# Optimization experiments

Measured on AMD Instinct MI355X. Metric: run time of the kernel, lower is better.

## Reference

```python
import math
import jax, jax.numpy as jnp
import numpy as np

N = 50000   # nodes
E = 200000  # edges
B = 1024    # graphs
D = 256     # d_model
DA = 128    # d_atom_embed
DB = 64     # d_bond_embed
NA = 16     # num_atom_types
NB = 5      # num_bond_types
L = 6       # num_layers
DC = 2      # d_cond
IN0 = DA + 8 + D  # 392, layer-0 input dim


def setup_inputs() -> dict:
    key = jax.random.key(0)
    ks = jax.random.split(key, 48)
    def w(i, shape):
        fan_in = shape[-2] if len(shape) >= 2 else shape[-1]
        return jax.random.normal(ks[i], shape, jnp.float32) / jnp.sqrt(jnp.float32(fan_in))
    inp = {
        'x_noisy': jax.random.randint(ks[0], (N,), 0, NA),
        'node_mask_obs': jax.random.randint(ks[1], (N,), 0, 2),
        'edge_attr_noisy': jax.random.randint(ks[2], (E,), 0, NB),
        'edge_mask_obs': jax.random.randint(ks[3], (E,), 0, 2),
        'edge_index': jax.random.randint(ks[4], (2, E), 0, N),
        't_node': jax.random.randint(ks[5], (N,), 0, 200),
        'cond_vec': jax.random.normal(ks[6], (B, DC), jnp.float32),
        'batch': jnp.sort(jax.random.randint(ks[7], (N,), 0, B)),
        # embeddings
        'atom_emb': w(8, (NA, DA)), 'bond_emb': w(9, (NB, DB)),
        'nmask_emb': w(10, (2, 8)), 'emask_emb': w(11, (2, 8)),
        # timestep MLP
        't_W1': w(12, (D, D)), 't_b1': jnp.zeros((D,)),
        't_W2': w(13, (D, D)), 't_b2': jnp.zeros((D,)),
        # cond projection
        'cond_W': w(14, (DC, D)), 'cond_b': jnp.zeros((D,)),
        # edge MLP
        'edge_W1': w(15, (DB + 8, D)), 'edge_b1': jnp.zeros((D,)),
        'edge_W2': w(16, (D, D)), 'edge_b2': jnp.zeros((D,)),
        # layer-0 edge projection (GINEConv edge_dim -> in_dim)
        'e0_W': w(17, (D, IN0)),
        # layer-0 GINEConv MLP
        'conv0_W1': w(18, (IN0, D)), 'conv0_b1': jnp.zeros((D,)),
        'conv0_W2': w(19, (D, D)), 'conv0_b2': jnp.zeros((D,)),
        'conv0_eps': jnp.zeros(()),
        # layers 1..5 GINEConv MLPs (stacked)
        'convs_W1': w(20, (L - 1, D, D)), 'convs_b1': jnp.zeros((L - 1, D)),
        'convs_W2': w(21, (L - 1, D, D)), 'convs_b2': jnp.zeros((L - 1, D)),
        'convs_eps': jnp.zeros((L - 1,)),
        # BatchNorm (eval mode: running_mean=0, running_var=1)
        'bn_gamma': jnp.ones((L, D)) + 0.1 * jax.random.normal(ks[22], (L, D), jnp.float32),
        'bn_beta': 0.1 * jax.random.normal(ks[23], (L, D), jnp.float32),
        # heads
        'atom_W': w(24, (D, NA)), 'atom_b': jnp.zeros((NA,)),
        'bond_W': w(25, (D, NB)), 'bond_b': jnp.zeros((NB,)),
    }
    return inp


def _sinusoidal(t, d_model):
    half = d_model // 2
    freqs = jnp.exp(jnp.arange(half, dtype=jnp.float32) * (-math.log(10000.0) / max(1, half - 1)))
    angles = t.astype(jnp.float32)[:, None] * freqs[None, :]
    return jnp.concatenate([jnp.sin(angles), jnp.cos(angles)], axis=1)


def _bn_eval(h, gamma, beta, eps=1e-5):
    # running_mean=0, running_var=1
    return h * (gamma / jnp.sqrt(1.0 + eps)) + beta


def reference(x_noisy, node_mask_obs, edge_attr_noisy, edge_mask_obs, edge_index,
              t_node, cond_vec, batch,
              atom_emb, bond_emb, nmask_emb, emask_emb,
              t_W1, t_b1, t_W2, t_b2, cond_W, cond_b,
              edge_W1, edge_b1, edge_W2, edge_b2, e0_W,
              conv0_W1, conv0_b1, conv0_W2, conv0_b2, conv0_eps,
              convs_W1, convs_b1, convs_W2, convs_b2, convs_eps,
              bn_gamma, bn_beta, atom_W, atom_b, bond_W, bond_b):
    silu = jax.nn.silu
    # node features
    x_atom = atom_emb[x_noisy]                       # [N, DA]
    x_mask = nmask_emb[node_mask_obs]                # [N, 8]
    t_emb = _sinusoidal(t_node, D)                   # [N, D]
    t_emb = silu(t_emb @ t_W1 + t_b1) @ t_W2 + t_b2
    c_node = (cond_vec @ cond_W + cond_b)[batch]     # [N, D]
    h = jnp.concatenate([x_atom, x_mask, t_emb + c_node], axis=-1)  # [N, IN0]
    # edge features
    e_in = jnp.concatenate([bond_emb[edge_attr_noisy], emask_emb[edge_mask_obs]], axis=-1)
    e_feat = silu(e_in @ edge_W1 + edge_b1) @ edge_W2 + edge_b2      # [E, D]
    src, dst = edge_index[0], edge_index[1]

    def gine(h, e, eps, W1, b1, W2, b2):
        msg = jax.nn.relu(h[src] + e)                               # [E, d]
        agg = jax.ops.segment_sum(msg, dst, num_segments=N)          # [N, d]
        z = (1.0 + eps) * h + agg
        return silu(z @ W1 + b1) @ W2 + b2

    # layer 0 (edge features projected to IN0)
    h = gine(h, e_feat @ e0_W, conv0_eps, conv0_W1, conv0_b1, conv0_W2, conv0_b2)
    h = silu(_bn_eval(h, bn_gamma[0], bn_beta[0]))  # dropout off (eval)
    # layers 1..5
    for i in range(L - 1):
        h = gine(h, e_feat, convs_eps[i], convs_W1[i], convs_b1[i], convs_W2[i], convs_b2[i])
        h = silu(_bn_eval(h, bn_gamma[i + 1], bn_beta[i + 1]))
    atom_logits = h @ atom_W + atom_b                # [N, NA]
    edge_h = h[src] + h[dst]                          # [E, D]
    bond_logits = edge_h @ bond_W + bond_b            # [E, NB]
    return atom_logits, bond_logits
```

## Files before the change

### kernel.cpp

```cpp
#include <hip/hip_runtime.h>
#include <cstdint>
#include <cmath>

typedef unsigned short u16;
typedef unsigned int   u32;

using bf16x8 = __attribute__((ext_vector_type(8))) short;
using f32x4  = __attribute__((ext_vector_type(4))) float;

#define DM 256
#define W0 448
#define W0_REAL 392

__device__ __forceinline__ float bf2f(u16 v) {
  union { u32 u; float f; } c; c.u = ((u32)v) << 16; return c.f;
}
__device__ __forceinline__ u16 f2bf(float f) {
  union { float f; u32 u; } c; c.f = f;
  u32 u = c.u;
  return (u16)((u + 0x7FFFu + ((u >> 16) & 1u)) >> 16);
}
__device__ __forceinline__ float siluf(float y) {
  return y / (1.0f + __expf(-y));
}
__device__ __forceinline__ uint4 pack8(float f0, float f1, float f2, float f3,
                                       float f4, float f5, float f6, float f7) {
  uint4 o;
  o.x = (u32)f2bf(f0) | ((u32)f2bf(f1) << 16);
  o.y = (u32)f2bf(f2) | ((u32)f2bf(f3) << 16);
  o.z = (u32)f2bf(f4) | ((u32)f2bf(f5) << 16);
  o.w = (u32)f2bf(f6) | ((u32)f2bf(f7) << 16);
  return o;
}
__device__ __forceinline__ void acc8(float4& lo, float4& hi, uint4 hv,
                                     float4 ea, float4 eb) {
  lo.x += fmaxf(bf2f((u16)(hv.x & 0xFFFF)) + ea.x, 0.f);
  lo.y += fmaxf(bf2f((u16)(hv.x >> 16))    + ea.y, 0.f);
  lo.z += fmaxf(bf2f((u16)(hv.y & 0xFFFF)) + ea.z, 0.f);
  lo.w += fmaxf(bf2f((u16)(hv.y >> 16))    + ea.w, 0.f);
  hi.x += fmaxf(bf2f((u16)(hv.z & 0xFFFF)) + eb.x, 0.f);
  hi.y += fmaxf(bf2f((u16)(hv.z >> 16))    + eb.y, 0.f);
  hi.z += fmaxf(bf2f((u16)(hv.w & 0xFFFF)) + eb.z, 0.f);
  hi.w += fmaxf(bf2f((u16)(hv.w >> 16))    + eb.w, 0.f);
}
__device__ __forceinline__ void g2l16(const u16* g, u16* l) {
  __builtin_amdgcn_global_load_lds(
      (__attribute__((address_space(1))) u32*)g,
      (__attribute__((address_space(3))) u32*)l, 16, 0, 0);
}

__global__ void wT_kernel(const float* __restrict__ W, u16* __restrict__ out,
                          int nmat, int K, int Kpad, int Nc) {
  int idx = blockIdx.x * 256 + threadIdx.x;
  int tot = nmat * Nc * Kpad;
  if (idx >= tot) return;
  int m = idx / (Nc * Kpad);
  int r = idx - m * (Nc * Kpad);
  int n = r / Kpad;
  int k = r - n * Kpad;
  float v = (k < K) ? W[(size_t)m * K * Nc + (size_t)k * Nc + n] : 0.0f;
  out[idx] = f2bf(v);
}

__global__ void whead_kernel(const float* __restrict__ atomW, const float* __restrict__ bondW,
                             u16* __restrict__ out) {
  int idx = blockIdx.x * 256 + threadIdx.x;
  if (idx >= 32 * 256) return;
  int j = idx >> 8, k = idx & 255;
  float v = 0.0f;
  if (j < 16) v = atomW[k * 16 + j];
  else if (j < 21) v = bondW[k * 5 + (j - 16)];
  out[idx] = f2bf(v);
}

__global__ void t_table_kernel(const float* __restrict__ W1, const float* __restrict__ b1,
                               const float* __restrict__ W2, const float* __restrict__ b2,
                               float* __restrict__ out) {
  __shared__ float s[256];
  __shared__ float a1[256];
  int r = blockIdx.x, t = threadIdx.x;
  float tv = (float)r;
  float coef = -logf(10000.0f) / 127.0f;
  int j = t & 127;
  float ang = tv * expf(coef * (float)j);
  s[t] = (t < 128) ? sinf(ang) : cosf(ang);
  __syncthreads();
  float acc = b1[t];
  for (int k = 0; k < 256; ++k) acc = fmaf(s[k], W1[k * 256 + t], acc);
  a1[t] = acc / (1.0f + expf(-acc));
  __syncthreads();
  float acc2 = b2[t];
  for (int k = 0; k < 256; ++k) acc2 = fmaf(a1[k], W2[k * 256 + t], acc2);
  out[r * 256 + t] = acc2;
}

__global__ void cproj_kernel(const float* __restrict__ cv, const float* __restrict__ W,
                             const float* __restrict__ b, float* __restrict__ out, int B) {
  int i = blockIdx.x * 256 + threadIdx.x;
  if (i < B * 256) {
    int g = i >> 8, c = i & 255;
    out[i] = fmaf(cv[g * 2], W[c], fmaf(cv[g * 2 + 1], W[256 + c], b[c]));
  }
}

__global__ void ef_tab_kernel(const float* __restrict__ bond_emb, const float* __restrict__ emask_emb,
                              const float* __restrict__ W1, const float* __restrict__ b1,
                              const float* __restrict__ W2, const float* __restrict__ b2,
                              float* __restrict__ out) {
  __shared__ float ein[72];
  __shared__ float a1[256];
  int bidx = blockIdx.x;
  int bt = bidx >> 1, m = bidx & 1;
  int t = threadIdx.x;
  if (t < 64) ein[t] = bond_emb[bt * 64 + t];
  else if (t < 72) ein[t] = emask_emb[m * 8 + (t - 64)];
  __syncthreads();
  float acc = b1[t];
  for (int k = 0; k < 72; ++k) acc = fmaf(ein[k], W1[k * 256 + t], acc);
  a1[t] = acc / (1.0f + expf(-acc));
  __syncthreads();
  float acc2 = b2[t];
  for (int k = 0; k < 256; ++k) acc2 = fmaf(a1[k], W2[k * 256 + t], acc2);
  out[bidx * 256 + t] = acc2;
}

__global__ void e0_tab_kernel(const float* __restrict__ eftab, const float* __restrict__ e0W,
                              float* __restrict__ out) {
  __shared__ float ef[256];
  int bidx = blockIdx.x, t = threadIdx.x;
  if (t < 256) ef[t] = eftab[bidx * 256 + t];
  __syncthreads();
  if (t < W0) {
    float acc = 0.0f;
    if (t < W0_REAL) {
      for (int k = 0; k < 256; ++k) acc = fmaf(ef[k], e0W[k * W0_REAL + t], acc);
    }
    out[bidx * W0 + t] = acc;
  }
}

__global__ void h0_kernel(const int* __restrict__ x, const int* __restrict__ nm,
                          const int* __restrict__ tnode, const int* __restrict__ batch,
                          const float* __restrict__ atom_emb, const float* __restrict__ nmask_emb,
                          const float* __restrict__ ttab, const float* __restrict__ cproj,
                          u16* __restrict__ h0, int N) {
  int idx = blockIdx.x * 256 + threadIdx.x;
  if (idx >= N * 56) return;
  int n = idx / 56;
  int ch = idx - n * 56;
  uint4 o;
  if (ch < 16) {
    const float* s = atom_emb + (size_t)x[n] * 128 + ch * 8;
    float4 a = *(const float4*)s, b = *(const float4*)(s + 4);
    o = pack8(a.x, a.y, a.z, a.w, b.x, b.y, b.z, b.w);
  } else if (ch == 16) {
    const float* s = nmask_emb + (size_t)nm[n] * 8;
    float4 a = *(const float4*)s, b = *(const float4*)(s + 4);
    o = pack8(a.x, a.y, a.z, a.w, b.x, b.y, b.z, b.w);
  } else if (ch < 49) {
    int cc = ch * 8 - 136;
    const float* ta = ttab + (size_t)tnode[n] * 256 + cc;
    const float* cb = cproj + (size_t)batch[n] * 256 + cc;
    float4 a = *(const float4*)ta, b = *(const float4*)(ta + 4);
    float4 c = *(const float4*)cb, d = *(const float4*)(cb + 4);
    o = pack8(a.x + c.x, a.y + c.y, a.z + c.z, a.w + c.w,
              b.x + d.x, b.y + d.y, b.z + d.z, b.w + d.w);
  } else {
    o = make_uint4(0, 0, 0, 0);
  }
  *(uint4*)(h0 + (size_t)n * W0 + ch * 8) = o;
}

__global__ void deg_kernel(const int* __restrict__ dst, int* __restrict__ deg, int E) {
  int e = blockIdx.x * 256 + threadIdx.x;
  if (e < E) atomicAdd(&deg[dst[e]], 1);
}

__global__ void scan1_kernel(const int* __restrict__ deg, int* __restrict__ ro,
                             int* __restrict__ bsum, int N) {
  __shared__ int tmp[256];
  int tid = threadIdx.x, i = blockIdx.x * 256 + tid;
  int v = (i < N) ? deg[i] : 0;
  tmp[tid] = v;
  __syncthreads();
  for (int o = 1; o < 256; o <<= 1) {
    int t = (tid >= o) ? tmp[tid - o] : 0;
    __syncthreads();
    tmp[tid] += t;
    __syncthreads();
  }
  if (i < N) ro[i] = tmp[tid] - v;
  if (tid == 255) bsum[blockIdx.x] = tmp[255];
}

__global__ void scan2_kernel(int* __restrict__ bsum, int nb) {
  __shared__ int tmp[256];
  int tid = threadIdx.x;
  int v = (tid < nb) ? bsum[tid] : 0;
  tmp[tid] = v;
  __syncthreads();
  for (int o = 1; o < 256; o <<= 1) {
    int t = (tid >= o) ? tmp[tid - o] : 0;
    __syncthreads();
    tmp[tid] += t;
    __syncthreads();
  }
  if (tid < nb) bsum[tid] = tmp[tid] - v;
}

__global__ void scan3_kernel(int* __restrict__ ro, int* __restrict__ cur,
                             const int* __restrict__ bsum, int N, int E) {
  int i = blockIdx.x * 256 + threadIdx.x;
  if (i < N) {
    int r = ro[i] + bsum[blockIdx.x];
    ro[i] = r;
    cur[i] = r;
  }
  if (i == 0) ro[N] = E;
}

__global__ void fill_kernel(const int* __restrict__ src, const int* __restrict__ dst,
                            const int* __restrict__ ea, const int* __restrict__ em,
                            int* __restrict__ cur, int* __restrict__ csr, int E) {
  int e = blockIdx.x * 256 + threadIdx.x;
  if (e < E) {
    int d = dst[e];
    int pos = atomicAdd(&cur[d], 1);
    csr[pos] = src[e] | ((ea[e] * 2 + em[e]) << 20);
  }
}

__global__ __launch_bounds__(256) void agg_z256(
    const u16* __restrict__ h, const float* __restrict__ etab,
    const int* __restrict__ ro, const int* __restrict__ csr,
    const float* __restrict__ epsp, u16* __restrict__ z, int N) {
  int wid = threadIdx.x >> 6, lane = threadIdx.x & 63;
  int n = blockIdx.x * 4 + wid;
  if (n >= N) return;
  int s0 = ro[n], s1 = ro[n + 1];
  float eps1 = 1.0f + *epsp;
  int half = lane >> 5, li = lane & 31;
  int c8 = li * 8;
  float4 aLo = {0, 0, 0, 0}, aHi = {0, 0, 0, 0};

  for (int base = s0; base < s1; base += 64) {
    int m = s1 - base; if (m > 64) m = 64;
    int pk = (lane < m) ? csr[base + lane] : 0;
    int j = 0;
    for (; j + 7 < m; j += 8) {
      int p0 = __shfl(pk, j + half);
      int p1 = __shfl(pk, j + 2 + half);
      int p2 = __shfl(pk, j + 4 + half);
      int p3 = __shfl(pk, j + 6 + half);
      uint4 h0v = *(const uint4*)(h + (size_t)(p0 & 0xFFFFF) * 256 + c8);
      uint4 h1v = *(const uint4*)(h + (size_t)(p1 & 0xFFFFF) * 256 + c8);
      uint4 h2v = *(const uint4*)(h + (size_t)(p2 & 0xFFFFF) * 256 + c8);
      uint4 h3v = *(const uint4*)(h + (size_t)(p3 & 0xFFFFF) * 256 + c8);
      const float* e0p = etab + (size_t)(p0 >> 20) * 256 + c8;
      const float* e1p = etab + (size_t)(p1 >> 20) * 256 + c8;
      const float* e2p = etab + (size_t)(p2 >> 20) * 256 + c8;
      const float* e3p = etab + (size_t)(p3 >> 20) * 256 + c8;
      float4 e0a = *(const float4*)e0p, e0b = *(const float4*)(e0p + 4);
      float4 e1a = *(const float4*)e1p, e1b = *(const float4*)(e1p + 4);
      float4 e2a = *(const float4*)e2p, e2b = *(const float4*)(e2p + 4);
      float4 e3a = *(const float4*)e3p, e3b = *(const float4*)(e3p + 4);
      acc8(aLo, aHi, h0v, e0a, e0b);
      acc8(aLo, aHi, h1v, e1a, e1b);
      acc8(aLo, aHi, h2v, e2a, e2b);
      acc8(aLo, aHi, h3v, e3a, e3b);
    }
    for (; j < m; j += 2) {
      int idx = j + half;
      bool act = idx < m;
      int p = __shfl(pk, act ? idx : (m - 1));
      uint4 hv = *(const uint4*)(h + (size_t)(p & 0xFFFFF) * 256 + c8);
      const float* ep = etab + (size_t)(p >> 20) * 256 + c8;
      float4 ea = *(const float4*)ep, eb = *(const float4*)(ep + 4);
      if (act) acc8(aLo, aHi, hv, ea, eb);
    }
  }
  aLo.x += __shfl(aLo.x, li + 32); aLo.y += __shfl(aLo.y, li + 32);
  aLo.z += __shfl(aLo.z, li + 32); aLo.w += __shfl(aLo.w, li + 32);
  aHi.x += __shfl(aHi.x, li + 32); aHi.y += __shfl(aHi.y, li + 32);
  aHi.z += __shfl(aHi.z, li + 32); aHi.w += __shfl(aHi.w, li + 32);
  if (half == 0) {
    uint4 hn = *(const uint4*)(h + (size_t)n * 256 + c8);
    uint4 o = pack8(
        eps1 * bf2f((u16)(hn.x & 0xFFFF)) + aLo.x,
        eps1 * bf2f((u16)(hn.x >> 16))    + aLo.y,
        eps1 * bf2f((u16)(hn.y & 0xFFFF)) + aLo.z,
        eps1 * bf2f((u16)(hn.y >> 16))    + aLo.w,
        eps1 * bf2f((u16)(hn.z & 0xFFFF)) + aHi.x,
        eps1 * bf2f((u16)(hn.z >> 16))    + aHi.y,
        eps1 * bf2f((u16)(hn.w & 0xFFFF)) + aHi.z,
        eps1 * bf2f((u16)(hn.w >> 16))    + aHi.w);
    *(uint4*)(z + (size_t)n * 256 + c8) = o;
  }
}

__global__ __launch_bounds__(256) void agg_z448(
    const u16* __restrict__ h, const float* __restrict__ etab,
    const int* __restrict__ ro, const int* __restrict__ csr,
    const float* __restrict__ epsp, u16* __restrict__ z, int N) {
  int wid = threadIdx.x >> 6, lane = threadIdx.x & 63;
  int n = blockIdx.x * 4 + wid;
  if (n >= N) return;
  int s0 = ro[n], s1 = ro[n + 1];
  float eps1 = 1.0f + *epsp;
  bool live = lane < 56;
  int c8 = live ? lane * 8 : 440;
  float4 aLo = {0, 0, 0, 0}, aHi = {0, 0, 0, 0};

  for (int base = s0; base < s1; base += 64) {
    int m = s1 - base; if (m > 64) m = 64;
    int pk = (lane < m) ? csr[base + lane] : 0;
    int j = 0;
    for (; j + 3 < m; j += 4) {
      int p0 = __shfl(pk, j);
      int p1 = __shfl(pk, j + 1);
      int p2 = __shfl(pk, j + 2);
      int p3 = __shfl(pk, j + 3);
      uint4 h0v = *(const uint4*)(h + (size_t)(p0 & 0xFFFFF) * W0 + c8);
      uint4 h1v = *(const uint4*)(h + (size_t)(p1 & 0xFFFFF) * W0 + c8);
      uint4 h2v = *(const uint4*)(h + (size_t)(p2 & 0xFFFFF) * W0 + c8);
      uint4 h3v = *(const uint4*)(h + (size_t)(p3 & 0xFFFFF) * W0 + c8);
      const float* e0p = etab + (size_t)(p0 >> 20) * W0 + c8;
      const float* e1p = etab + (size_t)(p1 >> 20) * W0 + c8;
      const float* e2p = etab + (size_t)(p2 >> 20) * W0 + c8;
      const float* e3p = etab + (size_t)(p3 >> 20) * W0 + c8;
      float4 e0a = *(const float4*)e0p, e0b = *(const float4*)(e0p + 4);
      float4 e1a = *(const float4*)e1p, e1b = *(const float4*)(e1p + 4);
      float4 e2a = *(const float4*)e2p, e2b = *(const float4*)(e2p + 4);
      float4 e3a = *(const float4*)e3p, e3b = *(const float4*)(e3p + 4);
      acc8(aLo, aHi, h0v, e0a, e0b);
      acc8(aLo, aHi, h1v, e1a, e1b);
      acc8(aLo, aHi, h2v, e2a, e2b);
      acc8(aLo, aHi, h3v, e3a, e3b);
    }
    for (; j < m; ++j) {
      int p = __shfl(pk, j);
      uint4 hv = *(const uint4*)(h + (size_t)(p & 0xFFFFF) * W0 + c8);
      const float* ep = etab + (size_t)(p >> 20) * W0 + c8;
      float4 ea = *(const float4*)ep, eb = *(const float4*)(ep + 4);
      acc8(aLo, aHi, hv, ea, eb);
    }
  }
  if (live) {
    uint4 hn = *(const uint4*)(h + (size_t)n * W0 + c8);
    uint4 o = pack8(
        eps1 * bf2f((u16)(hn.x & 0xFFFF)) + aLo.x,
        eps1 * bf2f((u16)(hn.x >> 16))    + aLo.y,
        eps1 * bf2f((u16)(hn.y & 0xFFFF)) + aLo.z,
        eps1 * bf2f((u16)(hn.y >> 16))    + aLo.w,
        eps1 * bf2f((u16)(hn.z & 0xFFFF)) + aHi.x,
        eps1 * bf2f((u16)(hn.z >> 16))    + aHi.y,
        eps1 * bf2f((u16)(hn.w & 0xFFFF)) + aHi.z,
        eps1 * bf2f((u16)(hn.w >> 16))    + aHi.w);
    *(uint4*)(z + (size_t)n * W0 + c8) = o;
  }
}

__global__ __launch_bounds__(256, 3) void gemm_fused(
    const u16* __restrict__ A, const u16* __restrict__ BT,
    const float* __restrict__ bias, const float* __restrict__ scale,
    const float* __restrict__ shift, u16* __restrict__ C, int M, int K) {
  __shared__ __align__(16) u16 smem[20480];
  u16* lA = smem;
  u16* lB = smem + 4096;
  int tid = threadIdx.x;
  int wid = tid >> 6, lane = tid & 63;
  int q = lane >> 4, rr = lane & 15;
  int wm = wid >> 1, wn = wid & 1;
  int m0 = blockIdx.x * 64;
  int lr8 = lane >> 3;
  int swz = (lane & 7) ^ (lr8 & 7);

  f32x4 acc[2][8] = {};

  for (int k0 = 0; k0 < K; k0 += 64) {
#pragma unroll
    for (int p = 0; p < 2; ++p) {
      int idx = wid * 2 + p;
      int gr = m0 + idx * 8 + lr8;
      if (gr >= M) gr = M - 1;
      g2l16(A + (size_t)gr * K + k0 + swz * 8, lA + idx * 512);
    }
#pragma unroll
    for (int p = 0; p < 8; ++p) {
      int idx = wid * 8 + p;
      int nr = idx * 8 + lr8;
      g2l16(BT + (size_t)nr * K + k0 + swz * 8, lB + idx * 512);
    }
    __syncthreads();
#pragma unroll
    for (int ks = 0; ks < 2; ++ks) {
      int slot = ((ks * 4 + q) ^ (rr & 7)) << 3;
      bf16x8 af[2], bfv[8];
#pragma unroll
      for (int mt = 0; mt < 2; ++mt)
        af[mt] = *(const bf16x8*)&lA[(wm * 32 + mt * 16 + rr) * 64 + slot];
#pragma unroll
      for (int nt = 0; nt < 8; ++nt)
        bfv[nt] = *(const bf16x8*)&lB[(wn * 128 + nt * 16 + rr) * 64 + slot];
#pragma unroll
      for (int mt = 0; mt < 2; ++mt)
#pragma unroll
        for (int nt = 0; nt < 8; ++nt)
          acc[mt][nt] = __builtin_amdgcn_mfma_f32_16x16x32_bf16(af[mt], bfv[nt], acc[mt][nt], 0, 0, 0);
    }
    __syncthreads();
  }

  u16* lC = smem;
#pragma unroll
  for (int nt = 0; nt < 8; ++nt) {
    int c = wn * 128 + nt * 16 + rr;
    float b = bias[c];
    float sc = scale ? scale[c] * 0.9999950000374997f : 1.0f;
    float sh = shift ? shift[c] : 0.0f;
#pragma unroll
    for (int mt = 0; mt < 2; ++mt)
#pragma unroll
      for (int i = 0; i < 4; ++i) {
        int r = wm * 32 + mt * 16 + q * 4 + i;
        float y = (acc[mt][nt][i] + b) * sc + sh;
        lC[r * 256 + c] = f2bf(siluf(y));
      }
  }
  __syncthreads();
#pragma unroll
  for (int it = 0; it < 8; ++it) {
    int idx = it * 256 + tid;
    int r = idx >> 5, c16 = idx & 31;
    if (m0 + r < M)
      *(uint4*)(C + (size_t)(m0 + r) * 256 + c16 * 8) =
          *(const uint4*)(lC + r * 256 + c16 * 8);
  }
}

__global__ __launch_bounds__(256) void head_gemm(
    const u16* __restrict__ A, const u16* __restrict__ WT,
    const float* __restrict__ atomB,
    float* __restrict__ atom_out, float* __restrict__ P, int M) {
  __shared__ __align__(16) u16 lA[128 * 32];
  __shared__ __align__(16) u16 lB[32 * 264];
  int tid = threadIdx.x;
  int wid = tid >> 6, lane = tid & 63;
  int q = lane >> 4, rr = lane & 15;
  int m0 = blockIdx.x * 128;

  for (int i = tid; i < 32 * 256; i += 256)
    lB[(i >> 8) * 264 + (i & 255)] = WT[i];

  f32x4 acc[2][2] = {};
  int arow = tid >> 2, acol = (tid & 3) * 8;

  for (int k0 = 0; k0 < 256; k0 += 32) {
#pragma unroll
    for (int p = 0; p < 2; ++p) {
      int gr = m0 + p * 64 + arow;
      if (gr >= M) gr = M - 1;
      g2l16(A + (size_t)gr * 256 + k0 + acol, &lA[p * 2048 + wid * 512]);
    }
    __syncthreads();
    bf16x8 af[2], bfr[2];
#pragma unroll
    for (int mt = 0; mt < 2; ++mt)
      af[mt] = *(const bf16x8*)&lA[(wid * 32 + mt * 16 + rr) * 32 + q * 8];
#pragma unroll
    for (int nt = 0; nt < 2; ++nt)
      bfr[nt] = *(const bf16x8*)&lB[(nt * 16 + rr) * 264 + k0 + q * 8];
#pragma unroll
    for (int mt = 0; mt < 2; ++mt)
#pragma unroll
      for (int nt = 0; nt < 2; ++nt)
        acc[mt][nt] = __builtin_amdgcn_mfma_f32_16x16x32_bf16(af[mt], bfr[nt], acc[mt][nt], 0, 0, 0);
    __syncthreads();
  }

#pragma unroll
  for (int nt = 0; nt < 2; ++nt) {
    int c = nt * 16 + rr;
    float bb = (c < 16) ? atomB[c] : 0.0f;
#pragma unroll
    for (int mt = 0; mt < 2; ++mt) {
      int rbase = m0 + wid * 32 + mt * 16 + q * 4;
#pragma unroll
      for (int r2 = 0; r2 < 4; ++r2) {
        int row = rbase + r2;
        if (row < M) {
          float v = acc[mt][nt][r2];
          if (c < 16) atom_out[(size_t)row * 16 + c] = v + bb;
          else if (c < 21) P[(size_t)row * 8 + (c - 16)] = v;
        }
      }
    }
  }
}

__global__ __launch_bounds__(256) void bond_edge(
    const float* __restrict__ P, const int* __restrict__ src,
    const int* __restrict__ dst, const float* __restrict__ b,
    float* __restrict__ out, int E) {
  __shared__ float so[256 * 5];
  int t = threadIdx.x;
  int e = blockIdx.x * 256 + t;
  float v0 = 0, v1 = 0, v2 = 0, v3 = 0, v4 = 0;
  if (e < E) {
    int s = src[e], d = dst[e];
    float4 ps = *(const float4*)(P + (size_t)s * 8);
    float  p4s = P[(size_t)s * 8 + 4];
    float4 pd = *(const float4*)(P + (size_t)d * 8);
    float  p4d = P[(size_t)d * 8 + 4];
    v0 = ps.x + pd.x + b[0];
    v1 = ps.y + pd.y + b[1];
    v2 = ps.z + pd.z + b[2];
    v3 = ps.w + pd.w + b[3];
    v4 = p4s + p4d + b[4];
  }
  so[t * 5 + 0] = v0; so[t * 5 + 1] = v1; so[t * 5 + 2] = v2;
  so[t * 5 + 3] = v3; so[t * 5 + 4] = v4;
  __syncthreads();
  size_t base = (size_t)blockIdx.x * 256 * 5;
  size_t lim = (size_t)E * 5;
  for (int i = t; i < 256 * 5; i += 256) {
    size_t g = base + i;
    if (g < lim) out[g] = so[i];
  }
}

extern "C" void kernel_launch(void* const* d_in, const int* in_sizes, int n_in,
                              void* d_out, int out_size, void* d_ws, size_t ws_size,
                              hipStream_t stream) {
  const int*   x_noisy   = (const int*)d_in[0];
  const int*   nmaskobs  = (const int*)d_in[1];
  const int*   ea        = (const int*)d_in[2];
  const int*   em        = (const int*)d_in[3];
  const int*   eidx      = (const int*)d_in[4];
  const int*   tnode     = (const int*)d_in[5];
  const float* cvec      = (const float*)d_in[6];
  const int*   batch     = (const int*)d_in[7];
  const float* atom_emb  = (const float*)d_in[8];
  const float* bond_emb  = (const float*)d_in[9];
  const float* nmask_emb = (const float*)d_in[10];
  const float* emask_emb = (const float*)d_in[11];
  const float* t_W1      = (const float*)d_in[12];
  const float* t_b1      = (const float*)d_in[13];
  const float* t_W2      = (const float*)d_in[14];
  const float* t_b2      = (const float*)d_in[15];
  const float* cond_W    = (const float*)d_in[16];
  const float* cond_b    = (const float*)d_in[17];
  const float* edge_W1   = (const float*)d_in[18];
  const float* edge_b1   = (const float*)d_in[19];
  const float* edge_W2   = (const float*)d_in[20];
  const float* edge_b2   = (const float*)d_in[21];
  const float* e0_W      = (const float*)d_in[22];
  const float* conv0_W1  = (const float*)d_in[23];
  const float* conv0_b1  = (const float*)d_in[24];
  const float* conv0_W2  = (const float*)d_in[25];
  const float* conv0_b2  = (const float*)d_in[26];
  const float* conv0_eps = (const float*)d_in[27];
  const float* convs_W1  = (const float*)d_in[28];
  const float* convs_b1  = (const float*)d_in[29];
  const float* convs_W2  = (const float*)d_in[30];
  const float* convs_b2  = (const float*)d_in[31];
  const float* convs_eps = (const float*)d_in[32];
  const float* bn_gamma  = (const float*)d_in[33];
  const float* bn_beta   = (const float*)d_in[34];
  const float* atom_W    = (const float*)d_in[35];
  const float* atom_b    = (const float*)d_in[36];
  const float* bond_W    = (const float*)d_in[37];
  const float* bond_b    = (const float*)d_in[38];

  const int N = in_sizes[0];
  const int E = in_sizes[2];
  const int B = in_sizes[6] / 2;
  const int* srcp = eidx;
  const int* dstp = eidx + E;

  char* base = (char*)d_ws;
  size_t off = 0;
  auto alloc = [&](size_t bytes) -> char* {
    char* p = base + off;
    off = (off + bytes + 255) & ~(size_t)255;
    return p;
  };
  u16* h0   = (u16*)alloc((size_t)N * W0 * 2);
  u16* z0   = (u16*)alloc((size_t)N * W0 * 2);
  u16* ubuf = (u16*)alloc((size_t)N * DM * 2);
  u16* w10t = (u16*)alloc((size_t)DM * W0 * 2);
  u16* w20t = (u16*)alloc((size_t)DM * DM * 2);
  u16* wc1t = (u16*)alloc((size_t)5 * DM * DM * 2);
  u16* wc2t = (u16*)alloc((size_t)5 * DM * DM * 2);
  u16* wht  = (u16*)alloc((size_t)32 * DM * 2);
  float* ttab  = (float*)alloc((size_t)200 * DM * 4);
  float* cprojb= (float*)alloc((size_t)B * DM * 4);
  float* eftab = (float*)alloc((size_t)10 * DM * 4);
  float* e0tab = (float*)alloc((size_t)10 * W0 * 4);
  float* Pbuf  = (float*)alloc((size_t)N * 8 * 4);
  int* deg  = (int*)alloc((size_t)N * 4);
  int* ro   = (int*)alloc((size_t)(N + 1) * 4);
  int* cur  = (int*)alloc((size_t)N * 4);
  int* csr  = (int*)alloc((size_t)E * 4);
  int* bsum = (int*)alloc((size_t)256 * 4);
  (void)ws_size; (void)n_in; (void)out_size;

  u16* hbuf = h0;
  u16* zbuf = z0;
  float* atom_out = (float*)d_out;
  float* bond_out = atom_out + (size_t)N * 16;

  hipMemsetAsync(deg, 0, (size_t)N * 4, stream);

  wT_kernel<<<(DM * W0 + 255) / 256, 256, 0, stream>>>(conv0_W1, w10t, 1, W0_REAL, W0, DM);
  wT_kernel<<<(DM * DM + 255) / 256, 256, 0, stream>>>(conv0_W2, w20t, 1, DM, DM, DM);
  wT_kernel<<<(5 * DM * DM + 255) / 256, 256, 0, stream>>>(convs_W1, wc1t, 5, DM, DM, DM);
  wT_kernel<<<(5 * DM * DM + 255) / 256, 256, 0, stream>>>(convs_W2, wc2t, 5, DM, DM, DM);
  whead_kernel<<<32, 256, 0, stream>>>(atom_W, bond_W, wht);
  t_table_kernel<<<200, 256, 0, stream>>>(t_W1, t_b1, t_W2, t_b2, ttab);
  cproj_kernel<<<(B * DM + 255) / 256, 256, 0, stream>>>(cvec, cond_W, cond_b, cprojb, B);
  ef_tab_kernel<<<10, 256, 0, stream>>>(bond_emb, emask_emb, edge_W1, edge_b1, edge_W2, edge_b2, eftab);
  e0_tab_kernel<<<10, 512, 0, stream>>>(eftab, e0_W, e0tab);
  h0_kernel<<<(N * 56 + 255) / 256, 256, 0, stream>>>(x_noisy, nmaskobs, tnode, batch,
      atom_emb, nmask_emb, ttab, cprojb, h0, N);
  const int nscan = (N + 255) / 256;
  deg_kernel<<<(E + 255) / 256, 256, 0, stream>>>(dstp, deg, E);
  scan1_kernel<<<nscan, 256, 0, stream>>>(deg, ro, bsum, N);
  scan2_kernel<<<1, 256, 0, stream>>>(bsum, nscan);
  scan3_kernel<<<nscan, 256, 0, stream>>>(ro, cur, bsum, N, E);
  fill_kernel<<<(E + 255) / 256, 256, 0, stream>>>(srcp, dstp, ea, em, cur, csr, E);

  const int ggrid = (N + 63) / 64;
  const int nagg = (N + 3) / 4;
  agg_z448<<<nagg, 256, 0, stream>>>(h0, e0tab, ro, csr, conv0_eps, z0, N);
  gemm_fused<<<ggrid, 256, 0, stream>>>(z0, w10t, conv0_b1, nullptr, nullptr, ubuf, N, W0);
  gemm_fused<<<ggrid, 256, 0, stream>>>(ubuf, w20t, conv0_b2, bn_gamma, bn_beta, hbuf, N, DM);
  for (int i = 0; i < 5; ++i) {
    agg_z256<<<nagg, 256, 0, stream>>>(hbuf, eftab, ro, csr, convs_eps + i, zbuf, N);
    gemm_fused<<<ggrid, 256, 0, stream>>>(zbuf, wc1t + (size_t)i * DM * DM, convs_b1 + i * DM,
                                          nullptr, nullptr, ubuf, N, DM);
    gemm_fused<<<ggrid, 256, 0, stream>>>(ubuf, wc2t + (size_t)i * DM * DM, convs_b2 + i * DM,
                                          bn_gamma + (i + 1) * DM, bn_beta + (i + 1) * DM, hbuf, N, DM);
  }
  head_gemm<<<(N + 127) / 128, 256, 0, stream>>>(hbuf, wht, atom_b, atom_out, Pbuf, N);
  bond_edge<<<(E + 255) / 256, 256, 0, stream>>>(Pbuf, srcp, dstp, bond_b, bond_out, E);
}
```

Baseline: 771.2 us.

## Fuse both GINE MLP GEMMs into one kernel with LDS-resident intermediate

The two back-to-back GEMMs of each GINE MLP are replaced with a single kernel that processes 128-row tiles. The intermediate SiLU activation stays in swizzled LDS instead of going through global memory, and the second GEMM reads it from LDS before applying the bias, BatchNorm and SiLU epilogue. Operands for the A and weight matrices are now loaded directly from global memory into registers rather than staged through LDS with async copies. This removes one launch and one round-trip of an N×256 buffer per layer, at the cost of 64 KB LDS per block, lower occupancy and unshared, uncoalesced weight loads.

```diff
diff --git a/kernel.cpp b/kernel.cpp
--- a/kernel.cpp
+++ b/kernel.cpp
@@ -42,6 +42,9 @@
   hi.y += fmaxf(bf2f((u16)(hv.z >> 16))    + eb.y, 0.f);
   hi.z += fmaxf(bf2f((u16)(hv.w & 0xFFFF)) + eb.z, 0.f);
   hi.w += fmaxf(bf2f((u16)(hv.w >> 16))    + eb.w, 0.f);
+}
+__device__ __forceinline__ int swzpos(int j, int r) {
+  return ((j & ~7) | ((j & 7) ^ (r & 7))) << 3;
 }
 __device__ __forceinline__ void g2l16(const u16* g, u16* l) {
   __builtin_amdgcn_global_load_lds(
@@ -360,81 +363,109 @@
   }
 }
 
-__global__ __launch_bounds__(256, 3) void gemm_fused(
-    const u16* __restrict__ A, const u16* __restrict__ BT,
-    const float* __restrict__ bias, const float* __restrict__ scale,
-    const float* __restrict__ shift, u16* __restrict__ C, int M, int K) {
-  __shared__ __align__(16) u16 smem[20480];
-  u16* lA = smem;
-  u16* lB = smem + 4096;
+__global__ __launch_bounds__(256, 2) void mlp_fused(
+    const u16* __restrict__ Z, int K1,
+    const u16* __restrict__ W1T, const float* __restrict__ b1,
+    const u16* __restrict__ W2T, const float* __restrict__ b2,
+    const float* __restrict__ gamma, const float* __restrict__ beta,
+    u16* __restrict__ hout, int M) {
+  __shared__ __align__(16) u16 uP[128 * 256];
   int tid = threadIdx.x;
   int wid = tid >> 6, lane = tid & 63;
   int q = lane >> 4, rr = lane & 15;
   int wm = wid >> 1, wn = wid & 1;
-  int m0 = blockIdx.x * 64;
-  int lr8 = lane >> 3;
-  int swz = (lane & 7) ^ (lr8 & 7);
-
-  f32x4 acc[2][8] = {};
-
-  for (int k0 = 0; k0 < K; k0 += 64) {
-#pragma unroll
-    for (int p = 0; p < 2; ++p) {
-      int idx = wid * 2 + p;
-      int gr = m0 + idx * 8 + lr8;
-      if (gr >= M) gr = M - 1;
-      g2l16(A + (size_t)gr * K + k0 + swz * 8, lA + idx * 512);
-    }
-#pragma unroll
-    for (int p = 0; p < 8; ++p) {
-      int idx = wid * 8 + p;
-      int nr = idx * 8 + lr8;
-      g2l16(BT + (size_t)nr * K + k0 + swz * 8, lB + idx * 512);
-    }
-    __syncthreads();
-#pragma unroll
-    for (int ks = 0; ks < 2; ++ks) {
-      int slot = ((ks * 4 + q) ^ (rr & 7)) << 3;
-      bf16x8 af[2], bfv[8];
-#pragma unroll
-      for (int mt = 0; mt < 2; ++mt)
-        af[mt] = *(const bf16x8*)&lA[(wm * 32 + mt * 16 + rr) * 64 + slot];
+  int m0 = blockIdx.x * 128;
+
+  int arow[4];
+#pragma unroll
+  for (int mt = 0; mt < 4; ++mt) {
+    int r = m0 + wm * 64 + mt * 16 + rr;
+    arow[mt] = (r < M) ? r : (M - 1);
+  }
+  int bcol[8];
+#pragma unroll
+  for (int nt = 0; nt < 8; ++nt) bcol[nt] = wn * 128 + nt * 16 + rr;
+
+  f32x4 acc[4][8];
+#pragma unroll
+  for (int mt = 0; mt < 4; ++mt)
+#pragma unroll
+    for (int nt = 0; nt < 8; ++nt) acc[mt][nt] = (f32x4){0, 0, 0, 0};
+  for (int k0 = 0; k0 < K1; k0 += 32) {
+    bf16x8 af[4], bv[8];
+#pragma unroll
+    for (int mt = 0; mt < 4; ++mt)
+      af[mt] = *(const bf16x8*)(Z + (size_t)arow[mt] * K1 + k0 + q * 8);
+#pragma unroll
+    for (int nt = 0; nt < 8; ++nt)
+      bv[nt] = *(const bf16x8*)(W1T + (size_t)bcol[nt] * K1 + k0 + q * 8);
+#pragma unroll
+    for (int mt = 0; mt < 4; ++mt)
 #pragma unroll
       for (int nt = 0; nt < 8; ++nt)
-        bfv[nt] = *(const bf16x8*)&lB[(wn * 128 + nt * 16 + rr) * 64 + slot];
-#pragma unroll
-      for (int mt = 0; mt < 2; ++mt)
-#pragma unroll
-        for (int nt = 0; nt < 8; ++nt)
-          acc[mt][nt] = __builtin_amdgcn_mfma_f32_16x16x32_bf16(af[mt], bfv[nt], acc[mt][nt], 0, 0, 0);
-    }
-    __syncthreads();
-  }
-
-  u16* lC = smem;
+        acc[mt][nt] = __builtin_amdgcn_mfma_f32_16x16x32_bf16(af[mt], bv[nt], acc[mt][nt], 0, 0, 0);
+  }
 #pragma unroll
   for (int nt = 0; nt < 8; ++nt) {
     int c = wn * 128 + nt * 16 + rr;
-    float b = bias[c];
-    float sc = scale ? scale[c] * 0.9999950000374997f : 1.0f;
-    float sh = shift ? shift[c] : 0.0f;
-#pragma unroll
-    for (int mt = 0; mt < 2; ++mt)
+    float bb = b1[c];
+    int j = c >> 3;
+#pragma unroll
+    for (int mt = 0; mt < 4; ++mt)
 #pragma unroll
       for (int i = 0; i < 4; ++i) {
-        int r = wm * 32 + mt * 16 + q * 4 + i;
-        float y = (acc[mt][nt][i] + b) * sc + sh;
-        lC[r * 256 + c] = f2bf(siluf(y));
+        int r = wm * 64 + mt * 16 + q * 4 + i;
+        uP[r * 256 + swzpos(j, r) + (c & 7)] = f2bf(siluf(acc[mt][nt][i] + bb));
       }
   }
   __syncthreads();
-#pragma unroll
-  for (int it = 0; it < 8; ++it) {
+
+#pragma unroll
+  for (int mt = 0; mt < 4; ++mt)
+#pragma unroll
+    for (int nt = 0; nt < 8; ++nt) acc[mt][nt] = (f32x4){0, 0, 0, 0};
+  for (int k0 = 0; k0 < 256; k0 += 32) {
+    int j0 = (k0 >> 3) + q;
+    bf16x8 af[4], bv[8];
+#pragma unroll
+    for (int mt = 0; mt < 4; ++mt) {
+      int r = wm * 64 + mt * 16 + rr;
+      af[mt] = *(const bf16x8*)&uP[r * 256 + swzpos(j0, r)];
+    }
+#pragma unroll
+    for (int nt = 0; nt < 8; ++nt)
+      bv[nt] = *(const bf16x8*)(W2T + (size_t)bcol[nt] * 256 + k0 + q * 8);
+#pragma unroll
+    for (int mt = 0; mt < 4; ++mt)
+#pragma unroll
+      for (int nt = 0; nt < 8; ++nt)
+        acc[mt][nt] = __builtin_amdgcn_mfma_f32_16x16x32_bf16(af[mt], bv[nt], acc[mt][nt], 0, 0, 0);
+  }
+  __syncthreads();
+
+#pragma unroll
+  for (int nt = 0; nt < 8; ++nt) {
+    int c = wn * 128 + nt * 16 + rr;
+    float bb = b2[c];
+    float sc = gamma[c] * 0.9999950000374997f;
+    float sh = beta[c];
+#pragma unroll
+    for (int mt = 0; mt < 4; ++mt)
+#pragma unroll
+      for (int i = 0; i < 4; ++i) {
+        int r = wm * 64 + mt * 16 + q * 4 + i;
+        float y = (acc[mt][nt][i] + bb) * sc + sh;
+        uP[r * 256 + c] = f2bf(siluf(y));
+      }
+  }
+  __syncthreads();
+#pragma unroll
+  for (int it = 0; it < 16; ++it) {
     int idx = it * 256 + tid;
-    int r = idx >> 5, c16 = idx & 31;
+    int r = idx >> 5, c8 = (idx & 31) * 8;
     if (m0 + r < M)
-      *(uint4*)(C + (size_t)(m0 + r) * 256 + c16 * 8) =
-          *(const uint4*)(lC + r * 256 + c16 * 8);
+      *(uint4*)(hout + (size_t)(m0 + r) * 256 + c8) =
+          *(const uint4*)(uP + r * 256 + c8);
   }
 }
 
@@ -586,8 +617,8 @@
     return p;
   };
   u16* h0   = (u16*)alloc((size_t)N * W0 * 2);
-  u16* z0   = (u16*)alloc((size_t)N * W0 * 2);
-  u16* ubuf = (u16*)alloc((size_t)N * DM * 2);
+  u16* zbuf = (u16*)alloc((size_t)N * W0 * 2);
+  u16* hbuf = (u16*)alloc((size_t)N * DM * 2);
   u16* w10t = (u16*)alloc((size_t)DM * W0 * 2);
   u16* w20t = (u16*)alloc((size_t)DM * DM * 2);
   u16* wc1t = (u16*)alloc((size_t)5 * DM * DM * 2);
@@ -605,8 +636,6 @@
   int* bsum = (int*)alloc((size_t)256 * 4);
   (void)ws_size; (void)n_in; (void)out_size;
 
-  u16* hbuf = h0;
-  u16* zbuf = z0;
   float* atom_out = (float*)d_out;
   float* bond_out = atom_out + (size_t)N * 16;
 
@@ -630,17 +659,17 @@
   scan3_kernel<<<nscan, 256, 0, stream>>>(ro, cur, bsum, N, E);
   fill_kernel<<<(E + 255) / 256, 256, 0, stream>>>(srcp, dstp, ea, em, cur, csr, E);
 
-  const int ggrid = (N + 63) / 64;
+  const int gmlp = (N + 127) / 128;
   const int nagg = (N + 3) / 4;
-  agg_z448<<<nagg, 256, 0, stream>>>(h0, e0tab, ro, csr, conv0_eps, z0, N);
-  gemm_fused<<<ggrid, 256, 0, stream>>>(z0, w10t, conv0_b1, nullptr, nullptr, ubuf, N, W0);
-  gemm_fused<<<ggrid, 256, 0, stream>>>(ubuf, w20t, conv0_b2, bn_gamma, bn_beta, hbuf, N, DM);
+  agg_z448<<<nagg, 256, 0, stream>>>(h0, e0tab, ro, csr, conv0_eps, zbuf, N);
+  mlp_fused<<<gmlp, 256, 0, stream>>>(zbuf, W0, w10t, conv0_b1, w20t, conv0_b2,
+                                      bn_gamma, bn_beta, hbuf, N);
   for (int i = 0; i < 5; ++i) {
     agg_z256<<<nagg, 256, 0, stream>>>(hbuf, eftab, ro, csr, convs_eps + i, zbuf, N);
-    gemm_fused<<<ggrid, 256, 0, stream>>>(zbuf, wc1t + (size_t)i * DM * DM, convs_b1 + i * DM,
-                                          nullptr, nullptr, ubuf, N, DM);
-    gemm_fused<<<ggrid, 256, 0, stream>>>(ubuf, wc2t + (size_t)i * DM * DM, convs_b2 + i * DM,
-                                          bn_gamma + (i + 1) * DM, bn_beta + (i + 1) * DM, hbuf, N, DM);
+    mlp_fused<<<gmlp, 256, 0, stream>>>(zbuf, DM,
+        wc1t + (size_t)i * DM * DM, convs_b1 + i * DM,
+        wc2t + (size_t)i * DM * DM, convs_b2 + i * DM,
+        bn_gamma + (i + 1) * DM, bn_beta + (i + 1) * DM, hbuf, N);
   }
   head_gemm<<<(N + 127) / 128, 256, 0, stream>>>(hbuf, wht, atom_b, atom_out, Pbuf, N);
   bond_edge<<<(E + 255) / 256, 256, 0, stream>>>(Pbuf, srcp, dstp, bond_b, bond_out, E);
```

New measurement: 805.9 us. +4.5%, slower.
